# Optimization experiments

Hardware: AMD Instinct MI355X
Metric: run time of the kernel (lower is better)

Reference implementation:

```python
import jax, jax.numpy as jnp
import numpy as np

LAYERS = 3       # opt.layer
B = 4096         # batch of sessions
MAX_LEN = 200    # padded session length
N_ITEMS = 100000 # item vocab (index 0 is PAD after zero-row concat)
E = 112          # emb_size (SessConv default)
EPS = 1e-12      # F.normalize eps


def setup_inputs() -> dict:
    key = jax.random.key(0)
    k0, k1, k2, k3, k4 = jax.random.split(key, 5)
    item_embedding = jax.random.normal(k0, (N_ITEMS, E), dtype=jnp.float32) * 0.1
    # Session-session adjacency A and diagonal inverse-degree D (so D @ A is row-normalized)
    A = jax.random.uniform(k1, (B, B), dtype=jnp.float32)
    D = jnp.diag(1.0 / A.sum(axis=1))
    # Padded session item indices; 0 == PAD row (zeros prepended to the table)
    session_item = jax.random.randint(k2, (B, MAX_LEN), 0, N_ITEMS + 1, dtype=jnp.int64)
    session_len = jax.random.randint(k3, (B, 1), 1, MAX_LEN + 1).astype(jnp.float32)
    # layers x Linear(E, E, bias=False) weights, torch layout [out, in]
    Ws = jax.random.normal(k4, (LAYERS, E, E), dtype=jnp.float32) * (1.0 / np.sqrt(E))
    return {"item_embedding": item_embedding, "D": D, "A": A,
            "session_len": session_len, "Ws": Ws, "session_item": session_item}


def reference(item_embedding, D, A, session_len, Ws, session_item):
    # Prepend zero row so index 0 gathers zeros (padding)
    emb = jnp.concatenate([jnp.zeros((1, E), item_embedding.dtype), item_embedding], axis=0)
    # Fused ragged gather + mean-pool (replaces per-session index_select + cpu/numpy roundtrip)
    seq_h = emb[session_item]                       # [B, MAX_LEN, E]
    session_emb = seq_h.sum(axis=1) / session_len   # [B, E]
    DA = D @ A                                      # [B, B]
    acc = session_emb                               # layer-0 term of the final average
    for i in range(LAYERS):
        session_emb = session_emb @ Ws[i].T         # Linear(E,E,bias=False)
        session_emb = DA @ session_emb              # session graph propagation
        nrm = jnp.linalg.norm(session_emb, axis=-1, keepdims=True)
        acc = acc + session_emb / jnp.maximum(nrm, EPS)  # appended term is L2-normalized
        # NOTE: next layer consumes the UN-normalized session_emb (as in the torch code)
    return acc / (LAYERS + 1)
```

## Files before the change

### kernel.cpp

```cpp
#include <hip/hip_runtime.h>
#include <hip/hip_bf16.h>

#define BSZ 4096
#define MAXLEN 200
#define EDIM 112
#define NPL 8

typedef __attribute__((ext_vector_type(8))) short bf16x8;
typedef __attribute__((ext_vector_type(4))) float f32x4;

static __device__ __forceinline__ short f2bf(float f) {
    unsigned u = __float_as_uint(f);
    unsigned r = (u + 0x7fffu + ((u >> 16) & 1u)) >> 16;
    return (short)r;
}
static __device__ __forceinline__ float bf2f(short s) {
    return __uint_as_float(((unsigned)(unsigned short)s) << 16);
}
static __device__ __forceinline__ bf16x8 cvt8(float4 a, float4 b) {
    bf16x8 r;
    r[0] = f2bf(a.x); r[1] = f2bf(a.y); r[2] = f2bf(a.z); r[3] = f2bf(a.w);
    r[4] = f2bf(b.x); r[5] = f2bf(b.y); r[6] = f2bf(b.z); r[7] = f2bf(b.w);
    return r;
}
static __device__ __forceinline__ unsigned pack2(float a, float b) {
    return ((unsigned)f2bf(a) & 0xffffu) | ((unsigned)f2bf(b) << 16);
}

static __device__ __forceinline__ void glds16(const unsigned short* g, unsigned short* l) {
    __builtin_amdgcn_global_load_lds(
        (__attribute__((address_space(1))) void*)(void*)g,
        (__attribute__((address_space(3))) void*)l, 16, 0, 0);
}

__global__ __launch_bounds__(256) void f32_to_bf16(const float* __restrict__ src,
                                                   unsigned short* __restrict__ dst,
                                                   int ngroups, int zgroups) {
    int g = blockIdx.x * 256 + threadIdx.x;
    if (g >= ngroups) return;
    bf16x8 o;
    if (g < zgroups) {
        #pragma unroll
        for (int i = 0; i < 8; ++i) o[i] = 0;
    } else {
        const float* p = src + (size_t)(g - zgroups) * 8;
        float4 a = *(const float4*)p;
        float4 b = *(const float4*)(p + 4);
        o = cvt8(a, b);
    }
    *(bf16x8*)(dst + (size_t)g * 8) = o;
}

__global__ __launch_bounds__(256) void gather_pool_bf(const unsigned short* __restrict__ Ebf,
                                                      const int* __restrict__ items,
                                                      const float* __restrict__ slen,
                                                      float* __restrict__ S,
                                                      float* __restrict__ acc) {
    __shared__ float part[16][14][8];
    int wave = threadIdx.x >> 6;
    int lane = threadIdx.x & 63;
    int b = blockIdx.x;
    int rg = lane / 14;
    int c  = lane % 14;
    const int* it = items + (size_t)b * MAXLEN + wave * 50;
    float a[8];
    #pragma unroll
    for (int e = 0; e < 8; ++e) a[e] = 0.f;
    if (lane < 56) {
        #pragma unroll
        for (int t = 0; t < 13; ++t) {
            int j = t * 4 + rg;
            int idx = 0;
            if (j < 50) idx = it[j];
            bf16x8 v = *(const bf16x8*)(Ebf + (size_t)idx * EDIM + c * 8);
            #pragma unroll
            for (int e = 0; e < 8; ++e) a[e] += bf2f(v[e]);
        }
        #pragma unroll
        for (int e = 0; e < 8; ++e) part[wave * 4 + rg][c][e] = a[e];
    }
    __syncthreads();
    int tid = threadIdx.x;
    if (tid < EDIM) {
        int cc = tid >> 3, ee = tid & 7;
        float s = 0.f;
        #pragma unroll
        for (int g = 0; g < 16; ++g) s += part[g][cc][ee];
        s /= slen[b];
        S[(size_t)b * EDIM + tid]   = s;
        acc[(size_t)b * EDIM + tid] = s;
    }
}

static __device__ __forceinline__ bf16x8 ldcvt(const float* p, bool valid) {
    if (valid) {
        float4 a = *(const float4*)(p);
        float4 b = *(const float4*)(p + 4);
        return cvt8(a, b);
    }
    bf16x8 z;
    #pragma unroll
    for (int i = 0; i < 8; ++i) z[i] = 0;
    return z;
}

__global__ __launch_bounds__(64, 4) void fused_mid0(const float* __restrict__ Sin,
                                                    const float* __restrict__ W,
                                                    unsigned short* __restrict__ Bsw) {
    __shared__ unsigned short Ylds[16][136];
    int lane = threadIdx.x;
    int gw = blockIdx.x;
    int j0 = gw * 16;
    int nrow = lane & 15;
    int quad = lane >> 4;
    int ses = j0 + nrow;

    float4 v[7];
    const float4* p = (const float4*)(Sin + (size_t)ses * EDIM + quad * 28);
    #pragma unroll
    for (int i = 0; i < 7; ++i) v[i] = p[i];

    #pragma unroll
    for (int i = 0; i < 7; ++i) {
        uint2 pk;
        pk.x = pack2(v[i].x, v[i].y);
        pk.y = pack2(v[i].z, v[i].w);
        *(uint2*)&Ylds[nrow][quad * 28 + i * 4] = pk;
    }
    *(uint2*)&Ylds[nrow][112 + quad * 4] = make_uint2(0u, 0u);
    __syncthreads();

    bf16x8 aF[4];
    #pragma unroll
    for (int k32 = 0; k32 < 4; ++k32)
        aF[k32] = *(bf16x8*)&Ylds[nrow][k32 * 32 + quad * 8];

    f32x4 acc[7];
    #pragma unroll
    for (int t = 0; t < 7; ++t) acc[t] = (f32x4){0.f, 0.f, 0.f, 0.f};
    #pragma unroll
    for (int t = 0; t < 7; ++t) {
        const float* wr = W + (size_t)(16 * t + nrow) * EDIM;
        #pragma unroll
        for (int k32 = 0; k32 < 4; ++k32) {
            bf16x8 bF = ldcvt(wr + k32 * 32 + quad * 8, (k32 < 3) || (quad < 2));
            acc[t] = __builtin_amdgcn_mfma_f32_16x16x32_bf16(aF[k32], bF, acc[t], 0, 0, 0);
        }
    }

    int k32f = j0 >> 5;
    int qp = ((j0 >> 4) & 1) * 2 + (quad >> 1);
    int e0 = (quad & 1) * 4;
    #pragma unroll
    for (int t = 0; t < 7; ++t) {
        uint2 pk;
        pk.x = pack2(acc[t][0], acc[t][1]);
        pk.y = pack2(acc[t][2], acc[t][3]);
        *(uint2*)(Bsw + ((size_t)(k32f * 7 + t) * 64 + qp * 16 + nrow) * 8 + e0) = pk;
    }
}

template <int AMODE>
__global__ __launch_bounds__(512, 2) void bg_m97(const float* __restrict__ Af,
                                                 unsigned short* __restrict__ Asw,
                                                 const unsigned short* __restrict__ Bsw,
                                                 float* __restrict__ Yp) {
    __shared__ unsigned short Ab[2][16 * 512];
    __shared__ unsigned short Bb[2][14 * 512];
    int tid = threadIdx.x;
    int w = tid >> 6;
    int lane = tid & 63;
    int nrow = lane & 15;
    int quad = lane >> 4;
    int mtile = blockIdx.x & 31;
    int kq = blockIdx.x >> 5;
    int M16 = mtile * 8 + w;

    f32x4 acc[7];
    #pragma unroll
    for (int t = 0; t < 7; ++t) acc[t] = (f32x4){0.f, 0.f, 0.f, 0.f};

    auto STAGE = [&](int s, int buf) {
        int k32b = kq * 16 + s * 2;
        #pragma unroll
        for (int j = 0; j < 2; ++j) {
            int f = w * 2 + j;
            size_t afrag = (((size_t)M16 * 128 + k32b + j) * 64 + lane) * 8;
            if (AMODE == 0) {
                const float* p = Af + (size_t)(M16 * 16 + nrow) * BSZ
                                 + (k32b + j) * 32 + quad * 8;
                float4 a0 = *(const float4*)p;
                float4 a1 = *(const float4*)(p + 4);
                bf16x8 r = cvt8(a0, a1);
                *(bf16x8*)&Ab[buf][f * 512 + lane * 8] = r;
                *(bf16x8*)(Asw + afrag) = r;
            } else {
                glds16(Asw + afrag, &Ab[buf][f * 512]);
            }
        }
        if (w < 7) {
            #pragma unroll
            for (int j = 0; j < 2; ++j) {
                int c = w * 2 + j;
                glds16(Bsw + (((size_t)k32b * 7 + c) * 64 + lane) * 8,
                       &Bb[buf][c * 512]);
            }
        }
    };

    STAGE(0, 0);
    __syncthreads();
    int cur = 0;
    #pragma unroll 1
    for (int s = 0; s < 8; ++s) {
        if (s < 7) STAGE(s + 1, cur ^ 1);
        #pragma unroll
        for (int kk = 0; kk < 2; ++kk) {
            bf16x8 aF = *(bf16x8*)&Ab[cur][(w * 2 + kk) * 512 + lane * 8];
            #pragma unroll
            for (int t = 0; t < 7; ++t) {
                bf16x8 bF = *(bf16x8*)&Bb[cur][(kk * 7 + t) * 512 + lane * 8];
                acc[t] = __builtin_amdgcn_mfma_f32_16x16x32_bf16(aF, bF, acc[t], 0, 0, 0);
            }
        }
        __syncthreads();
        cur ^= 1;
    }

    float* dst = Yp + (size_t)kq * BSZ * EDIM + (size_t)(M16 * 16) * EDIM;
    #pragma unroll
    for (int t = 0; t < 7; ++t)
        #pragma unroll
        for (int r = 0; r < 4; ++r)
            dst[(size_t)(quad * 4 + r) * EDIM + 16 * t + nrow] = acc[t][r];
}

__global__ __launch_bounds__(64, 4) void epi_mid(const float* __restrict__ Yp,
                                                 const float* __restrict__ Dm,
                                                 float* __restrict__ accb,
                                                 const float* __restrict__ W,
                                                 unsigned short* __restrict__ Bsw) {
    __shared__ unsigned short Ylds[16][136];
    int lane = threadIdx.x;
    int gw = blockIdx.x;
    int j0 = gw * 16;
    int nrow = lane & 15;
    int quad = lane >> 4;
    int ses = j0 + nrow;

    float4 v[7];
    #pragma unroll
    for (int i = 0; i < 7; ++i) v[i] = make_float4(0.f, 0.f, 0.f, 0.f);
    #pragma unroll
    for (int pp = 0; pp < NPL; ++pp) {
        const float4* p = (const float4*)(Yp + (size_t)pp * BSZ * EDIM
                                          + (size_t)ses * EDIM + quad * 28);
        #pragma unroll
        for (int i = 0; i < 7; ++i) {
            float4 t = p[i];
            v[i].x += t.x; v[i].y += t.y; v[i].z += t.z; v[i].w += t.w;
        }
    }
    float d = Dm[(size_t)ses * (BSZ + 1)];
    float ss = 0.f;
    #pragma unroll
    for (int i = 0; i < 7; ++i) {
        v[i].x *= d; v[i].y *= d; v[i].z *= d; v[i].w *= d;
        ss += v[i].x * v[i].x + v[i].y * v[i].y + v[i].z * v[i].z + v[i].w * v[i].w;
    }
    ss += __shfl_xor(ss, 16, 64);
    ss += __shfl_xor(ss, 32, 64);
    float rinv = 1.f / fmaxf(sqrtf(ss), 1e-12f);
    float4* pa = (float4*)(accb + (size_t)ses * EDIM + quad * 28);
    #pragma unroll
    for (int i = 0; i < 7; ++i) {
        float4 a = pa[i];
        a.x += v[i].x * rinv; a.y += v[i].y * rinv;
        a.z += v[i].z * rinv; a.w += v[i].w * rinv;
        pa[i] = a;
    }

    #pragma unroll
    for (int i = 0; i < 7; ++i) {
        uint2 pk;
        pk.x = pack2(v[i].x, v[i].y);
        pk.y = pack2(v[i].z, v[i].w);
        *(uint2*)&Ylds[nrow][quad * 28 + i * 4] = pk;
    }
    *(uint2*)&Ylds[nrow][112 + quad * 4] = make_uint2(0u, 0u);
    __syncthreads();

    bf16x8 aF[4];
    #pragma unroll
    for (int k32 = 0; k32 < 4; ++k32)
        aF[k32] = *(bf16x8*)&Ylds[nrow][k32 * 32 + quad * 8];

    f32x4 acc[7];
    #pragma unroll
    for (int t = 0; t < 7; ++t) acc[t] = (f32x4){0.f, 0.f, 0.f, 0.f};
    #pragma unroll
    for (int t = 0; t < 7; ++t) {
        const float* wr = W + (size_t)(16 * t + nrow) * EDIM;
        #pragma unroll
        for (int k32 = 0; k32 < 4; ++k32) {
            bf16x8 bF = ldcvt(wr + k32 * 32 + quad * 8, (k32 < 3) || (quad < 2));
            acc[t] = __builtin_amdgcn_mfma_f32_16x16x32_bf16(aF[k32], bF, acc[t], 0, 0, 0);
        }
    }

    int k32f = j0 >> 5;
    int qp = ((j0 >> 4) & 1) * 2 + (quad >> 1);
    int e0 = (quad & 1) * 4;
    #pragma unroll
    for (int t = 0; t < 7; ++t) {
        uint2 pk;
        pk.x = pack2(acc[t][0], acc[t][1]);
        pk.y = pack2(acc[t][2], acc[t][3]);
        *(uint2*)(Bsw + ((size_t)(k32f * 7 + t) * 64 + qp * 16 + nrow) * 8 + e0) = pk;
    }
}

__global__ __launch_bounds__(256) void final_epilogue(const float* __restrict__ Yp,
                                                      const float* __restrict__ Dm,
                                                      const float* __restrict__ accb,
                                                      float* __restrict__ out) {
    int wave = threadIdx.x >> 6;
    int lane = threadIdx.x & 63;
    int b = blockIdx.x * 4 + wave;

    float2 v = make_float2(0.f, 0.f);
    size_t o2 = (size_t)b * 56 + lane;
    if (lane < 56) {
        #pragma unroll
        for (int p = 0; p < NPL; ++p) {
            float2 t = ((const float2*)(Yp + (size_t)p * BSZ * EDIM))[o2];
            v.x += t.x;
            v.y += t.y;
        }
    }
    float d = Dm[(size_t)b * (BSZ + 1)];
    v.x *= d; v.y *= d;
    float ss = v.x * v.x + v.y * v.y;
    #pragma unroll
    for (int off = 32; off; off >>= 1) ss += __shfl_xor(ss, off, 64);
    float nrm = fmaxf(sqrtf(ss), 1e-12f);
    if (lane < 56) {
        float2 a = ((const float2*)accb)[o2];
        ((float2*)out)[o2] = make_float2((a.x + v.x / nrm) * 0.25f,
                                         (a.y + v.y / nrm) * 0.25f);
    }
}

extern "C" void kernel_launch(void* const* d_in, const int* in_sizes, int n_in,
                              void* d_out, int out_size, void* d_ws, size_t ws_size,
                              hipStream_t stream) {
    (void)in_sizes; (void)n_in; (void)out_size; (void)ws_size;
    const float* emb   = (const float*)d_in[0];
    const float* Dm    = (const float*)d_in[1];
    const float* A     = (const float*)d_in[2];
    const float* slen  = (const float*)d_in[3];
    const float* Ws    = (const float*)d_in[4];
    const int*   items = (const int*)d_in[5];
    float* out = (float*)d_out;

    char* w = (char*)d_ws;
    float* Sa   = (float*)w;
    float* accb = Sa + BSZ * EDIM;
    float* Yp   = accb + BSZ * EDIM;
    unsigned short* Bsw0 = (unsigned short*)(Yp + (size_t)NPL * BSZ * EDIM);
    unsigned short* Bsw1 = Bsw0 + (size_t)128 * 7 * 64 * 8;
    unsigned short* Ebf  = Bsw1 + (size_t)128 * 7 * 64 * 8;
    unsigned short* Asw  = Ebf + (size_t)100001 * EDIM;

    f32_to_bf16<<<5470, 256, 0, stream>>>(emb, Ebf, 1400014, 14);
    gather_pool_bf<<<BSZ, 256, 0, stream>>>(Ebf, items, slen, Sa, accb);
    fused_mid0<<<256, 64, 0, stream>>>(Sa, Ws, Bsw0);
    bg_m97<0><<<256, 512, 0, stream>>>(A, Asw, Bsw0, Yp);
    epi_mid<<<256, 64, 0, stream>>>(Yp, Dm, accb, Ws + (size_t)EDIM * EDIM, Bsw1);
    bg_m97<1><<<256, 512, 0, stream>>>(nullptr, Asw, Bsw1, Yp);
    epi_mid<<<256, 64, 0, stream>>>(Yp, Dm, accb, Ws + (size_t)2 * EDIM * EDIM, Bsw0);
    bg_m97<1><<<256, 512, 0, stream>>>(nullptr, Asw, Bsw0, Yp);
    final_epilogue<<<BSZ / 4, 256, 0, stream>>>(Yp, Dm, accb, out);
}
```

Baseline: 276.7 us.

## Split A conversion into its own kernel and deepen GEMM load pipeline

Moves the fp32-to-bf16 swizzled conversion of A out of the first GEMM into a standalone cvtA kernel, so all three GEMM launches share one template that only does async global-to-LDS loads. The GEMM now stages one k32 slice per step into a 4-deep ring buffer, prefetching three stages ahead with explicit vmcnt waits and a raw barrier instead of double-buffered __syncthreads. The intent is to hide load latency better and simplify the first GEMM. In exchange it adds an extra kernel launch and an extra pass over A, and drops the occupancy hint from 2 blocks per CU to 1.

```diff
diff --git a/kernel.cpp b/kernel.cpp
--- a/kernel.cpp
+++ b/kernel.cpp
@@ -49,6 +49,21 @@
         o = cvt8(a, b);
     }
     *(bf16x8*)(dst + (size_t)g * 8) = o;
+}
+
+__global__ __launch_bounds__(256) void cvtA(const float* __restrict__ Af,
+                                            unsigned short* __restrict__ Asw) {
+    int tid = threadIdx.x;
+    int lane = tid & 63;
+    int sub = tid >> 6;
+    int blk = blockIdx.x;
+    int M16 = blk >> 5;
+    int k32 = (blk & 31) * 4 + sub;
+    int nrow = lane & 15, quad = lane >> 4;
+    const float* p = Af + (size_t)(M16 * 16 + nrow) * BSZ + k32 * 32 + quad * 8;
+    float4 a0 = *(const float4*)p;
+    float4 a1 = *(const float4*)(p + 4);
+    *(bf16x8*)(Asw + (((size_t)M16 * 128 + k32) * 64 + lane) * 8) = cvt8(a0, a1);
 }
 
 __global__ __launch_bounds__(256) void gather_pool_bf(const unsigned short* __restrict__ Ebf,
@@ -160,13 +175,11 @@
     }
 }
 
-template <int AMODE>
-__global__ __launch_bounds__(512, 2) void bg_m97(const float* __restrict__ Af,
-                                                 unsigned short* __restrict__ Asw,
-                                                 const unsigned short* __restrict__ Bsw,
-                                                 float* __restrict__ Yp) {
-    __shared__ unsigned short Ab[2][16 * 512];
-    __shared__ unsigned short Bb[2][14 * 512];
+__global__ __launch_bounds__(512, 1) void bg_pipe(const unsigned short* __restrict__ Asw,
+                                                  const unsigned short* __restrict__ Bsw,
+                                                  float* __restrict__ Yp) {
+    __shared__ unsigned short Ab[4][8 * 512];
+    __shared__ unsigned short Bb[4][8 * 512];
     int tid = threadIdx.x;
     int w = tid >> 6;
     int lane = tid & 63;
@@ -181,50 +194,31 @@
     for (int t = 0; t < 7; ++t) acc[t] = (f32x4){0.f, 0.f, 0.f, 0.f};
 
     auto STAGE = [&](int s, int buf) {
-        int k32b = kq * 16 + s * 2;
-        #pragma unroll
-        for (int j = 0; j < 2; ++j) {
-            int f = w * 2 + j;
-            size_t afrag = (((size_t)M16 * 128 + k32b + j) * 64 + lane) * 8;
-            if (AMODE == 0) {
-                const float* p = Af + (size_t)(M16 * 16 + nrow) * BSZ
-                                 + (k32b + j) * 32 + quad * 8;
-                float4 a0 = *(const float4*)p;
-                float4 a1 = *(const float4*)(p + 4);
-                bf16x8 r = cvt8(a0, a1);
-                *(bf16x8*)&Ab[buf][f * 512 + lane * 8] = r;
-                *(bf16x8*)(Asw + afrag) = r;
-            } else {
-                glds16(Asw + afrag, &Ab[buf][f * 512]);
-            }
-        }
-        if (w < 7) {
-            #pragma unroll
-            for (int j = 0; j < 2; ++j) {
-                int c = w * 2 + j;
-                glds16(Bsw + (((size_t)k32b * 7 + c) * 64 + lane) * 8,
-                       &Bb[buf][c * 512]);
-            }
-        }
+        int k32 = kq * 16 + s;
+        glds16(Asw + (((size_t)M16 * 128 + k32) * 64 + lane) * 8,
+               &Ab[buf][w * 512]);
+        int c = (w < 7) ? w : 0;
+        glds16(Bsw + (((size_t)k32 * 7 + c) * 64 + lane) * 8,
+               &Bb[buf][w * 512]);
     };
 
     STAGE(0, 0);
-    __syncthreads();
-    int cur = 0;
-    #pragma unroll 1
-    for (int s = 0; s < 8; ++s) {
-        if (s < 7) STAGE(s + 1, cur ^ 1);
-        #pragma unroll
-        for (int kk = 0; kk < 2; ++kk) {
-            bf16x8 aF = *(bf16x8*)&Ab[cur][(w * 2 + kk) * 512 + lane * 8];
-            #pragma unroll
-            for (int t = 0; t < 7; ++t) {
-                bf16x8 bF = *(bf16x8*)&Bb[cur][(kk * 7 + t) * 512 + lane * 8];
-                acc[t] = __builtin_amdgcn_mfma_f32_16x16x32_bf16(aF, bF, acc[t], 0, 0, 0);
-            }
-        }
-        __syncthreads();
-        cur ^= 1;
+    STAGE(1, 1);
+    STAGE(2, 2);
+    #pragma unroll
+    for (int s = 0; s < 16; ++s) {
+        if (s < 14)      asm volatile("s_waitcnt vmcnt(4)" ::: "memory");
+        else if (s == 14) asm volatile("s_waitcnt vmcnt(2)" ::: "memory");
+        else             asm volatile("s_waitcnt vmcnt(0)" ::: "memory");
+        __builtin_amdgcn_s_barrier();
+        if (s < 13) STAGE(s + 3, (s + 3) & 3);
+        int cur = s & 3;
+        bf16x8 aF = *(bf16x8*)&Ab[cur][w * 512 + lane * 8];
+        #pragma unroll
+        for (int t = 0; t < 7; ++t) {
+            bf16x8 bF = *(bf16x8*)&Bb[cur][t * 512 + lane * 8];
+            acc[t] = __builtin_amdgcn_mfma_f32_16x16x32_bf16(aF, bF, acc[t], 0, 0, 0);
+        }
     }
 
     float* dst = Yp + (size_t)kq * BSZ * EDIM + (size_t)(M16 * 16) * EDIM;
@@ -374,11 +368,12 @@
 
     f32_to_bf16<<<5470, 256, 0, stream>>>(emb, Ebf, 1400014, 14);
     gather_pool_bf<<<BSZ, 256, 0, stream>>>(Ebf, items, slen, Sa, accb);
+    cvtA<<<8192, 256, 0, stream>>>(A, Asw);
     fused_mid0<<<256, 64, 0, stream>>>(Sa, Ws, Bsw0);
-    bg_m97<0><<<256, 512, 0, stream>>>(A, Asw, Bsw0, Yp);
+    bg_pipe<<<256, 512, 0, stream>>>(Asw, Bsw0, Yp);
     epi_mid<<<256, 64, 0, stream>>>(Yp, Dm, accb, Ws + (size_t)EDIM * EDIM, Bsw1);
-    bg_m97<1><<<256, 512, 0, stream>>>(nullptr, Asw, Bsw1, Yp);
+    bg_pipe<<<256, 512, 0, stream>>>(Asw, Bsw1, Yp);
     epi_mid<<<256, 64, 0, stream>>>(Yp, Dm, accb, Ws + (size_t)2 * EDIM * EDIM, Bsw0);
-    bg_m97<1><<<256, 512, 0, stream>>>(nullptr, Asw, Bsw0, Yp);
+    bg_pipe<<<256, 512, 0, stream>>>(Asw, Bsw0, Yp);
     final_epilogue<<<BSZ / 4, 256, 0, stream>>>(Yp, Dm, accb, out);
 }
```

Result: no change. 274.0 us (-1.0%).

## Hold A fragments in registers and load B in two halves for the propagation GEMM

Applied to the files above, without the earlier changes.

The double-buffered 8-stage LDS pipeline in the DA-propagation GEMM is replaced. Each wave now loads all 16 of its A fragments straight into registers, with the fp32 convert-and-store in mode 0 or a direct bf16 load in mode 1. B is staged into LDS in two 8-k32 halves, so the loop needs far fewer barriers and A no longer passes through LDS. The cost is much higher register pressure (16 bf16x8 fragments per lane) and a hard vmcnt(0) wait before any compute, so load latency no longer overlaps with MFMA work inside a block.

```diff
diff --git a/kernel.cpp b/kernel.cpp
--- a/kernel.cpp
+++ b/kernel.cpp
@@ -161,12 +161,11 @@
 }
 
 template <int AMODE>
-__global__ __launch_bounds__(512, 2) void bg_m97(const float* __restrict__ Af,
-                                                 unsigned short* __restrict__ Asw,
-                                                 const unsigned short* __restrict__ Bsw,
-                                                 float* __restrict__ Yp) {
-    __shared__ unsigned short Ab[2][16 * 512];
-    __shared__ unsigned short Bb[2][14 * 512];
+__global__ __launch_bounds__(512, 2) void bg_ks(const float* __restrict__ Af,
+                                                unsigned short* __restrict__ Asw,
+                                                const unsigned short* __restrict__ Bsw,
+                                                float* __restrict__ Yp) {
+    __shared__ unsigned short Bl[8 * 7 * 512];
     int tid = threadIdx.x;
     int w = tid >> 6;
     int lane = tid & 63;
@@ -175,59 +174,62 @@
     int mtile = blockIdx.x & 31;
     int kq = blockIdx.x >> 5;
     int M16 = mtile * 8 + w;
+    int k32b = kq * 16;
+
+    #pragma unroll
+    for (int t = 0; t < 7; ++t)
+        glds16(Bsw + (((size_t)(k32b + w) * 7 + t) * 64 + lane) * 8,
+               &Bl[(w * 7 + t) * 512]);
+
+    bf16x8 aF[16];
+    if (AMODE == 0) {
+        #pragma unroll
+        for (int k = 0; k < 16; ++k) {
+            const float* p = Af + (size_t)(M16 * 16 + nrow) * BSZ
+                             + (k32b + k) * 32 + quad * 8;
+            float4 a0 = *(const float4*)p;
+            float4 a1 = *(const float4*)(p + 4);
+            aF[k] = cvt8(a0, a1);
+            *(bf16x8*)(Asw + (((size_t)M16 * 128 + k32b + k) * 64 + lane) * 8) = aF[k];
+        }
+    } else {
+        #pragma unroll
+        for (int k = 0; k < 16; ++k)
+            aF[k] = *(const bf16x8*)(Asw + (((size_t)M16 * 128 + k32b + k) * 64 + lane) * 8);
+    }
 
     f32x4 acc[7];
     #pragma unroll
     for (int t = 0; t < 7; ++t) acc[t] = (f32x4){0.f, 0.f, 0.f, 0.f};
 
-    auto STAGE = [&](int s, int buf) {
-        int k32b = kq * 16 + s * 2;
-        #pragma unroll
-        for (int j = 0; j < 2; ++j) {
-            int f = w * 2 + j;
-            size_t afrag = (((size_t)M16 * 128 + k32b + j) * 64 + lane) * 8;
-            if (AMODE == 0) {
-                const float* p = Af + (size_t)(M16 * 16 + nrow) * BSZ
-                                 + (k32b + j) * 32 + quad * 8;
-                float4 a0 = *(const float4*)p;
-                float4 a1 = *(const float4*)(p + 4);
-                bf16x8 r = cvt8(a0, a1);
-                *(bf16x8*)&Ab[buf][f * 512 + lane * 8] = r;
-                *(bf16x8*)(Asw + afrag) = r;
-            } else {
-                glds16(Asw + afrag, &Ab[buf][f * 512]);
-            }
-        }
-        if (w < 7) {
-            #pragma unroll
-            for (int j = 0; j < 2; ++j) {
-                int c = w * 2 + j;
-                glds16(Bsw + (((size_t)k32b * 7 + c) * 64 + lane) * 8,
-                       &Bb[buf][c * 512]);
-            }
-        }
-    };
-
-    STAGE(0, 0);
-    __syncthreads();
-    int cur = 0;
-    #pragma unroll 1
-    for (int s = 0; s < 8; ++s) {
-        if (s < 7) STAGE(s + 1, cur ^ 1);
-        #pragma unroll
-        for (int kk = 0; kk < 2; ++kk) {
-            bf16x8 aF = *(bf16x8*)&Ab[cur][(w * 2 + kk) * 512 + lane * 8];
-            #pragma unroll
-            for (int t = 0; t < 7; ++t) {
-                bf16x8 bF = *(bf16x8*)&Bb[cur][(kk * 7 + t) * 512 + lane * 8];
-                acc[t] = __builtin_amdgcn_mfma_f32_16x16x32_bf16(aF, bF, acc[t], 0, 0, 0);
-            }
-        }
-        __syncthreads();
-        cur ^= 1;
-    }
-
-    float* dst = Yp + (size_t)kq * BSZ * EDIM + (size_t)(M16 * 16) * EDIM;
+    asm volatile("s_waitcnt vmcnt(0)" ::: "memory");
+    __syncthreads();
+
+    #pragma unroll
+    for (int k = 0; k < 8; ++k)
+        #pragma unroll
+        for (int t = 0; t < 7; ++t) {
+            bf16x8 bF = *(bf16x8*)&Bl[(k * 7 + t) * 512 + lane * 8];
+            acc[t] = __builtin_amdgcn_mfma_f32_16x16x32_bf16(aF[k], bF, acc[t], 0, 0, 0);
+        }
+
+    __syncthreads();
+    #pragma unroll
+    for (int t = 0; t < 7; ++t)
+        glds16(Bsw + (((size_t)(k32b + 8 + w) * 7 + t) * 64 + lane) * 8,
+               &Bl[(w * 7 + t) * 512]);
+    asm volatile("s_waitcnt vmcnt(0)" ::: "memory");
+    __syncthreads();
+
+    #pragma unroll
+    for (int k = 0; k < 8; ++k)
+        #pragma unroll
+        for (int t = 0; t < 7; ++t) {
+            bf16x8 bF = *(bf16x8*)&Bl[(k * 7 + t) * 512 + lane * 8];
+            acc[t] = __builtin_amdgcn_mfma_f32_16x16x32_bf16(aF[8 + k], bF, acc[t], 0, 0, 0);
+        }
+
+    float* dst = Yp + (size_t)kq * BSZ * EDIM + (size_t)M16 * 16 * EDIM;
     #pragma unroll
     for (int t = 0; t < 7; ++t)
         #pragma unroll
@@ -375,10 +377,10 @@
     f32_to_bf16<<<5470, 256, 0, stream>>>(emb, Ebf, 1400014, 14);
     gather_pool_bf<<<BSZ, 256, 0, stream>>>(Ebf, items, slen, Sa, accb);
     fused_mid0<<<256, 64, 0, stream>>>(Sa, Ws, Bsw0);
-    bg_m97<0><<<256, 512, 0, stream>>>(A, Asw, Bsw0, Yp);
+    bg_ks<0><<<256, 512, 0, stream>>>(A, Asw, Bsw0, Yp);
     epi_mid<<<256, 64, 0, stream>>>(Yp, Dm, accb, Ws + (size_t)EDIM * EDIM, Bsw1);
-    bg_m97<1><<<256, 512, 0, stream>>>(nullptr, Asw, Bsw1, Yp);
+    bg_ks<1><<<256, 512, 0, stream>>>(nullptr, Asw, Bsw1, Yp);
     epi_mid<<<256, 64, 0, stream>>>(Yp, Dm, accb, Ws + (size_t)2 * EDIM * EDIM, Bsw0);
-    bg_m97<1><<<256, 512, 0, stream>>>(nullptr, Asw, Bsw0, Yp);
+    bg_ks<1><<<256, 512, 0, stream>>>(nullptr, Asw, Bsw0, Yp);
     final_epilogue<<<BSZ / 4, 256, 0, stream>>>(Yp, Dm, accb, out);
 }
```

Measured after the change: 274.3 us. About the same (-0.9%).
